# Performance work log

Hardware: AMD Instinct MI355X
Metric: run time of the kernel (lower is better)

## Reference

```python
import math
import jax, jax.numpy as jnp
import numpy as np

B, S, HID, NH = 2, 2048, 2048, 16
HD = HID // NH          # 128
QKD = HD // 2           # 64
BASE = 10000.0
LAYER_ID = 1
LAMBDA_INIT = 0.8 - 0.6 * math.exp(-0.3 * LAYER_ID)
EPS = 1e-6


def _rope_tables():
    i = np.arange(0, HD, 2, dtype=np.float32)
    theta = BASE ** (-i / HD)                      # [HD/2]
    pos = np.arange(S, dtype=np.float32)
    m_theta = np.outer(pos, theta)                 # [S, HD/2]
    cos = np.repeat(np.cos(m_theta), 2, axis=1)    # [S, HD]
    sin = np.repeat(np.sin(m_theta), 2, axis=1)
    return jnp.asarray(cos), jnp.asarray(sin)


def setup_inputs() -> dict:
    key = jax.random.key(0)
    ks = jax.random.split(key, 12)
    wstd = 0.02
    cos_emb, sin_emb = _rope_tables()
    return {
        "q": jax.random.normal(ks[0], (B, S, HID), jnp.float32),
        "k": jax.random.normal(ks[1], (B, S, HID), jnp.float32),
        "v": jax.random.normal(ks[2], (B, S, HID), jnp.float32),
        "Wq": jax.random.normal(ks[3], (HID, HID), jnp.float32) * wstd,
        "Wk": jax.random.normal(ks[4], (HID, HID), jnp.float32) * wstd,
        "Wv": jax.random.normal(ks[5], (HID, HID), jnp.float32) * wstd,
        "Wo": jax.random.normal(ks[6], (HID, HID), jnp.float32) * wstd,
        "lambda_q1": jax.random.normal(ks[7], (HD,), jnp.float32) * 0.1,
        "lambda_k1": jax.random.normal(ks[8], (HD,), jnp.float32) * 0.1,
        "lambda_q2": jax.random.normal(ks[9], (HD,), jnp.float32) * 0.1,
        "lambda_k2": jax.random.normal(ks[10], (HD,), jnp.float32) * 0.1,
        "gnorm_w": jnp.ones((HD,), jnp.float32),
        "cos_emb": cos_emb,
        "sin_emb": sin_emb,
        "mask": jnp.triu(jnp.ones((S, S), bool), 1),  # causal: True = masked
    }


def _apply_rope(x, cos_emb, sin_emb):
    # x: [B, 2, H, S, QKD]; tables sliced to [:S, :QKD] as in the torch code
    cos = cos_emb[:S, :QKD][None, None, None]
    sin = sin_emb[:S, :QKD][None, None, None]
    inv = jnp.stack((-x[..., 1::2], x[..., 0::2]), axis=-1).reshape(x.shape)
    return x * cos + inv * sin


def reference(q, k, v, Wq, Wk, Wv, Wo, lambda_q1, lambda_k1, lambda_q2,
              lambda_k2, gnorm_w, cos_emb, sin_emb, mask):
    lin = lambda x, W: jnp.einsum('bsi,oi->bso', x, W)  # torch Linear: x @ W.T
    qh = lin(q, Wq).reshape(B, S, NH, 2, QKD).transpose(0, 3, 2, 1, 4)  # [B,2,H,S,QKD]
    kh = lin(k, Wk).reshape(B, S, NH, 2, QKD).transpose(0, 3, 2, 1, 4)
    vh = lin(v, Wv).reshape(B, S, NH, HD).transpose(0, 2, 1, 3)          # [B,H,S,HD]
    qh = _apply_rope(qh, cos_emb, sin_emb)
    kh = _apply_rope(kh, cos_emb, sin_emb)

    scores = jnp.einsum('bghsd,bghtd->bghst', qh, kh) / math.sqrt(QKD)   # [B,2,H,S,S]
    scores = jnp.where(mask, jnp.finfo(jnp.float32).min, scores)

    lam1 = jnp.exp(jnp.sum(lambda_q1 * lambda_k1))
    lam2 = jnp.exp(jnp.sum(lambda_q2 * lambda_k2))
    lam = lam1 - lam2 + LAMBDA_INIT

    attn = jax.nn.softmax(scores[:, 0], axis=-1) - lam * jax.nn.softmax(scores[:, 1], axis=-1)
    out = jnp.einsum('bhst,bhtd->bhsd', attn, vh)                        # [B,H,S,HD]

    rms = out * jax.lax.rsqrt(jnp.mean(out * out, axis=-1, keepdims=True) + EPS) * gnorm_w
    out = (1.0 - LAMBDA_INIT) * rms
    out = out.transpose(0, 2, 1, 3).reshape(B, S, HID)
    return lin(out, Wo)
```

## Files before the change

kernel.cpp:

```cpp
#include <hip/hip_runtime.h>
#include <math.h>

#define BDIM 2
#define SDIM 2048
#define HIDD 2048
#define NHH 16
#define HDD 128
#define QKDD 64
#define MTOT (BDIM*SDIM)

constexpr float LAMBDA_INIT_F = 0.3555090675909693f;
constexpr float EPS_F = 1e-6f;
constexpr float SCALE2_F = 0.18033688011112042f;

typedef float f32x4 __attribute__((ext_vector_type(4)));
typedef short bf16x8 __attribute__((ext_vector_type(8)));
typedef short bf16x4 __attribute__((ext_vector_type(4)));

#define MFMA16(a, b, c) __builtin_amdgcn_mfma_f32_16x16x32_bf16((a), (b), (c), 0, 0, 0)

__device__ __forceinline__ short f2bf(float f) {
    unsigned u = __float_as_uint(f);
    u += 0x7FFFu + ((u >> 16) & 1u);
    return (short)(u >> 16);
}
__device__ __forceinline__ unsigned pk2(float a, float b) {
    return (unsigned)(unsigned short)f2bf(a) | ((unsigned)(unsigned short)f2bf(b) << 16);
}
__device__ __forceinline__ unsigned cvtpk(float lo, float hi) {
    unsigned r;
    asm("v_cvt_pk_bf16_f32 %0, %1, %2" : "=v"(r) : "v"(lo), "v"(hi));
    return r;
}

__device__ __forceinline__ void gload_lds16(const void* g, void* l) {
    __builtin_amdgcn_global_load_lds(
        (const __attribute__((address_space(1))) void*)g,
        (__attribute__((address_space(3))) void*)l, 16, 0, 0);
}
__device__ __forceinline__ void waitv8() { asm volatile("s_waitcnt vmcnt(8)" ::: "memory"); }
__device__ __forceinline__ void waitv0() { asm volatile("s_waitcnt vmcnt(0)" ::: "memory"); }
__device__ __forceinline__ void waitl0() { asm volatile("s_waitcnt lgkmcnt(0)" ::: "memory"); }
#define SBAR()   __builtin_amdgcn_s_barrier()
#define SCHEDB() __builtin_amdgcn_sched_barrier(0)

__global__ void lambda_kernel(const float* __restrict__ lq1, const float* __restrict__ lk1,
                              const float* __restrict__ lq2, const float* __restrict__ lk2,
                              float* __restrict__ lam_out) {
    int l = threadIdx.x;
    float d1 = lq1[l] * lk1[l] + lq1[l + 64] * lk1[l + 64];
    float d2 = lq2[l] * lk2[l] + lq2[l + 64] * lk2[l + 64];
#pragma unroll
    for (int o = 32; o > 0; o >>= 1) {
        d1 += __shfl_down(d1, o);
        d2 += __shfl_down(d2, o);
    }
    if (l == 0) lam_out[0] = expf(d1) - expf(d2) + LAMBDA_INIT_F;
}

__global__ __launch_bounds__(256) void conv_all(
        const float* __restrict__ q, const float* __restrict__ k,
        const float* __restrict__ v, const float* __restrict__ Wq,
        const float* __restrict__ Wk, const float* __restrict__ Wv,
        const float* __restrict__ Wo, short* __restrict__ xdst,
        short* __restrict__ wdst) {
    const size_t TEN_C = (size_t)1 << 23;
    const size_t WN_C  = (size_t)1 << 22;
    size_t i = ((size_t)blockIdx.x * 256 + threadIdx.x) * 8;
    const float* src;
    short* dst;
    size_t off;
    if (i < 3 * TEN_C) {
        int y = (int)(i >> 23);
        off = i & (TEN_C - 1);
        src = (y == 0) ? q : (y == 1) ? k : v;
        dst = xdst + ((size_t)y << 23);
    } else {
        size_t j = i - 3 * TEN_C;
        int y = (int)(j >> 22);
        off = j & (WN_C - 1);
        src = (y == 0) ? Wq : (y == 1) ? Wk : (y == 2) ? Wv : Wo;
        dst = wdst + ((size_t)y << 22);
    }
    float4 a = *(const float4*)&src[off];
    float4 b = *(const float4*)&src[off + 4];
    uint4 o;
    o.x = pk2(a.x, a.y); o.y = pk2(a.z, a.w);
    o.z = pk2(b.x, b.y); o.w = pk2(b.z, b.w);
    *(uint4*)&dst[off] = o;
}

#define GK 2048

__device__ __forceinline__ void gemm_mainloop(
        const short* __restrict__ X, const short* __restrict__ W,
        short* As, short* Bs, f32x4 acc[4][4],
        int bm, int bn, int w, int l, int lq, int lg, int wr, int wc) {
    const int scol = (((l & 7) ^ (l >> 3)) << 3);
    const int rsw  = (lq & 7) << 3;
    const short* aS[4]; const short* bS[4];
#pragma unroll
    for (int i = 0; i < 4; ++i) {
        const int c = w * 4 + i;
        aS[i] = X + (size_t)(bm + c * 8 + (l >> 3)) * GK + scol;
        bS[i] = W + (size_t)(bn + c * 8 + (l >> 3)) * GK + scol;
    }
    const int dOff = (w * 4) * 512;

#pragma unroll
    for (int i = 0; i < 4; ++i) {
        gload_lds16(aS[i], As + dOff + i * 512);
        gload_lds16(bS[i], Bs + dOff + i * 512);
    }
#pragma unroll
    for (int i = 0; i < 4; ++i) {
        gload_lds16(aS[i] + 64, As + 8192 + dOff + i * 512);
        gload_lds16(bS[i] + 64, Bs + 8192 + dOff + i * 512);
    }
    waitv8();
    SBAR();

    for (int t = 0; t < 30; ++t) {
        const short* Ab = As + (t & 1) * 8192;
        const short* Bb = Bs + (t & 1) * 8192;
        bf16x8 a[4][2], b[4][2];
#pragma unroll
        for (int m = 0; m < 4; ++m)
#pragma unroll
            for (int kk = 0; kk < 2; ++kk)
                a[m][kk] = *(const bf16x8*)&Ab[(wr * 64 + m * 16 + lq) * 64 + ((kk * 32 + lg * 8) ^ rsw)];
#pragma unroll
        for (int n = 0; n < 4; ++n)
#pragma unroll
            for (int kk = 0; kk < 2; ++kk)
                b[n][kk] = *(const bf16x8*)&Bb[(wc * 64 + n * 16 + lq) * 64 + ((kk * 32 + lg * 8) ^ rsw)];
        waitl0(); SCHEDB();
        SBAR();
        {
            short* Ad = As + (t & 1) * 8192 + dOff;
            short* Bd = Bs + (t & 1) * 8192 + dOff;
#pragma unroll
            for (int i = 0; i < 4; ++i) {
                gload_lds16(aS[i] + (t + 2) * 64, Ad + i * 512);
                gload_lds16(bS[i] + (t + 2) * 64, Bd + i * 512);
            }
        }
        SCHEDB();
#pragma unroll
        for (int kk = 0; kk < 2; ++kk)
#pragma unroll
            for (int m = 0; m < 4; ++m)
#pragma unroll
                for (int n = 0; n < 4; ++n)
                    acc[m][n] = MFMA16(a[m][kk], b[n][kk], acc[m][n]);
        waitv8();
        SBAR();
    }
    {
        bf16x8 a[4][2], b[4][2];
#pragma unroll
        for (int m = 0; m < 4; ++m)
#pragma unroll
            for (int kk = 0; kk < 2; ++kk)
                a[m][kk] = *(const bf16x8*)&As[(wr * 64 + m * 16 + lq) * 64 + ((kk * 32 + lg * 8) ^ rsw)];
#pragma unroll
        for (int n = 0; n < 4; ++n)
#pragma unroll
            for (int kk = 0; kk < 2; ++kk)
                b[n][kk] = *(const bf16x8*)&Bs[(wc * 64 + n * 16 + lq) * 64 + ((kk * 32 + lg * 8) ^ rsw)];
        waitl0(); SCHEDB();
        SBAR();
#pragma unroll
        for (int kk = 0; kk < 2; ++kk)
#pragma unroll
            for (int m = 0; m < 4; ++m)
#pragma unroll
                for (int n = 0; n < 4; ++n)
                    acc[m][n] = MFMA16(a[m][kk], b[n][kk], acc[m][n]);
        waitv0();
        SBAR();
    }
    {
        bf16x8 a[4][2], b[4][2];
#pragma unroll
        for (int m = 0; m < 4; ++m)
#pragma unroll
            for (int kk = 0; kk < 2; ++kk)
                a[m][kk] = *(const bf16x8*)&As[8192 + (wr * 64 + m * 16 + lq) * 64 + ((kk * 32 + lg * 8) ^ rsw)];
#pragma unroll
        for (int n = 0; n < 4; ++n)
#pragma unroll
            for (int kk = 0; kk < 2; ++kk)
                b[n][kk] = *(const bf16x8*)&Bs[8192 + (wc * 64 + n * 16 + lq) * 64 + ((kk * 32 + lg * 8) ^ rsw)];
#pragma unroll
        for (int kk = 0; kk < 2; ++kk)
#pragma unroll
            for (int m = 0; m < 4; ++m)
#pragma unroll
                for (int n = 0; n < 4; ++n)
                    acc[m][n] = MFMA16(a[m][kk], b[n][kk], acc[m][n]);
    }
}

__global__ __launch_bounds__(256) void qkv_gemm(
        const short* __restrict__ Xq, const short* __restrict__ Xk, const short* __restrict__ Xv,
        const short* __restrict__ Wb, short* __restrict__ Qb, short* __restrict__ Kb,
        short* __restrict__ Vb, const float* __restrict__ cosE, const float* __restrict__ sinE) {
    __shared__ short As[2 * 128 * 64];
    __shared__ short Bs[2 * 128 * 64];
    const int tid = threadIdx.x;
    const int w = tid >> 6, l = tid & 63;
    const int lq = l & 15, lg = l >> 4;
    const int wr = w >> 1, wc = w & 1;
    const int bm = blockIdx.y * 128;
    const int bn = blockIdx.x * 128;
    const int z  = blockIdx.z;

    const short* X = (z == 0) ? Xq : (z == 1) ? Xk : Xv;
    const short* W = Wb + (size_t)z * HIDD * HIDD;
    short* Cb      = (z == 0) ? Qb : (z == 1) ? Kb : Vb;

    f32x4 acc[4][4] = {};
    gemm_mainloop(X, W, As, Bs, acc, bm, bn, w, l, lq, lg, wr, wc);

    const bool dorope = (z < 2);
#pragma unroll
    for (int m = 0; m < 4; ++m)
#pragma unroll
        for (int n = 0; n < 4; ++n) {
            const int row0 = bm + wr * 64 + m * 16 + lg * 4;
            const int col  = bn + wc * 64 + n * 16 + lq;
#pragma unroll
            for (int r = 0; r < 4; ++r) {
                float vv = acc[m][n][r];
                if (dorope) {
                    const int s  = (row0 + r) & (SDIM - 1);
                    const int c6 = col & 63;
                    const float cv = cosE[s * HDD + c6];
                    const float sv = sinE[s * HDD + c6];
                    const float p = __shfl_xor(vv, 1);
                    vv = (col & 1) ? vv * cv + p * sv : vv * cv - p * sv;
                }
                Cb[(size_t)(row0 + r) * HIDD + col] = f2bf(vv);
            }
        }
}

__global__ __launch_bounds__(256) void o_gemm(const short* __restrict__ Ab,
                                              const short* __restrict__ Bb,
                                              float* __restrict__ C) {
    __shared__ short As[2 * 128 * 64];
    __shared__ short Bs[2 * 128 * 64];
    const int tid = threadIdx.x;
    const int w = tid >> 6, l = tid & 63;
    const int lq = l & 15, lg = l >> 4;
    const int wr = w >> 1, wc = w & 1;
    const int bm = blockIdx.y * 128;
    const int bn = blockIdx.x * 128;

    f32x4 acc[4][4] = {};
    gemm_mainloop(Ab, Bb, As, Bs, acc, bm, bn, w, l, lq, lg, wr, wc);

#pragma unroll
    for (int m = 0; m < 4; ++m)
#pragma unroll
        for (int n = 0; n < 4; ++n) {
            const int row0 = bm + wr * 64 + m * 16 + lg * 4;
            const int col  = bn + wc * 64 + n * 16 + lq;
#pragma unroll
            for (int r = 0; r < 4; ++r)
                C[(size_t)(row0 + r) * HIDD + col] = acc[m][n][r];
        }
}

#define KVB 64

__device__ __forceinline__ bf16x8 pack_pa(const float p0[4], const float p1[4]) {
    union { unsigned u[4]; bf16x8 v; } r;
    r.u[0] = cvtpk(p0[0], p0[1]);
    r.u[1] = cvtpk(p0[2], p0[3]);
    r.u[2] = cvtpk(p1[0], p1[1]);
    r.u[3] = cvtpk(p1[2], p1[3]);
    return r.v;
}

__device__ __forceinline__ void softmax_step(
        f32x4 sc[4], float& M, float& L, f32x4 O[8], bf16x8 pa[2],
        int t0, int qg, int lg, bool domask) {
#pragma unroll
    for (int sub = 0; sub < 4; ++sub)
#pragma unroll
        for (int r = 0; r < 4; ++r) {
            float s = sc[sub][r] * SCALE2_F;
            if (domask) {
                int key = t0 + sub * 16 + lg * 4 + r;
                s = (key <= qg) ? s : -1e30f;
            }
            sc[sub][r] = s;
        }
    float mx = -1e30f;
#pragma unroll
    for (int sub = 0; sub < 4; ++sub) {
        float a01 = fmaxf(sc[sub][0], sc[sub][1]);
        float a23 = fmaxf(sc[sub][2], sc[sub][3]);
        mx = fmaxf(mx, fmaxf(a01, a23));
    }
    mx = fmaxf(mx, __shfl_xor(mx, 16));
    mx = fmaxf(mx, __shfl_xor(mx, 32));
    if (__ballot(mx > M + 8.f)) {
        const float Mn = fmaxf(M, mx);
        const float a = __builtin_amdgcn_exp2f(M - Mn);
        M = Mn;
        L *= a;
        float ar[4];
#pragma unroll
        for (int r = 0; r < 4; ++r) ar[r] = __shfl(a, lg * 4 + r);
#pragma unroll
        for (int d = 0; d < 8; ++d) {
            O[d][0] *= ar[0]; O[d][1] *= ar[1]; O[d][2] *= ar[2]; O[d][3] *= ar[3];
        }
    }
    float p[4][4];
    float ps = 0.f;
#pragma unroll
    for (int sub = 0; sub < 4; ++sub) {
#pragma unroll
        for (int r = 0; r < 4; ++r) p[sub][r] = __builtin_amdgcn_exp2f(sc[sub][r] - M);
        ps += (p[sub][0] + p[sub][1]) + (p[sub][2] + p[sub][3]);
    }
    ps += __shfl_xor(ps, 16);
    ps += __shfl_xor(ps, 32);
    L += ps;
    pa[0] = pack_pa(p[0], p[1]);
    pa[1] = pack_pa(p[2], p[3]);
}

__global__ __launch_bounds__(256, 2) void flash_mfma(
        const short* __restrict__ Qb, const short* __restrict__ Kb,
        const short* __restrict__ Vb, const float* __restrict__ gnw,
        const float* __restrict__ lam_p, short* __restrict__ Hob) {
    __shared__ short Ksh[KVB * 128];
    __shared__ short VT[HDD * 72];

    const int tid = threadIdx.x;
    const int w  = tid >> 6;
    const int l  = tid & 63;
    const int lq = l & 15;
    const int lg = l >> 4;

    const int blk = blockIdx.x;
    const int bh  = blk & 31;
    const int g   = blk >> 5;
    const int r4  = g >> 3, gc = g & 7;
    const int bx  = (r4 == 0) ? 31 - gc : (r4 == 1) ? gc
                  : (r4 == 2) ? 23 - gc : 8 + gc;
    const int b = bh >> 4, h = bh & 15;
    const int s0 = bx * 64;
    const float lam = lam_p[0];

    const int qg = s0 + w * 16 + lq;
    const short* qrow = Qb + ((size_t)(b * SDIM + qg)) * HIDD + h * HDD;
    bf16x8 qf[2][2];
#pragma unroll
    for (int br = 0; br < 2; ++br)
#pragma unroll
        for (int ks = 0; ks < 2; ++ks)
            qf[br][ks] = *(const bf16x8*)(qrow + br * 64 + ks * 32 + lg * 8);

    int kkey[4], kcol[4];
#pragma unroll
    for (int i = 0; i < 4; ++i) {
        kkey[i] = w * 16 + i * 4 + lg;
        kcol[i] = (lq * 8) ^ ((kkey[i] & 7) << 3);
    }
    const int kp = tid & 31, dq = tid >> 5;

    const short* Kbase = Kb + ((size_t)(b * SDIM)) * HIDD + h * HDD;
    const short* Vbase = Vb + ((size_t)(b * SDIM)) * HIDD + h * HDD;

    float M1 = -1e30f, M2 = -1e30f, L1 = 0.f, L2 = 0.f;
    f32x4 O1[8] = {}; f32x4 O2[8] = {};

    const int ntmax = bx + 1;
    const int qmin = s0 + w * 16;

    for (int t = 0; t < ntmax; ++t) {
        const size_t trow = (size_t)t * KVB * HIDD;
        __syncthreads();
#pragma unroll
        for (int i = 0; i < 4; ++i)
            gload_lds16(Kbase + trow + (size_t)kkey[i] * HIDD + kcol[i],
                        &Ksh[w * 2048 + i * 512]);
        {
            const short* v0 = Vbase + trow + (size_t)(2 * kp) * HIDD + dq * 16;
            const short* v1 = v0 + HIDD;
            bf16x8 v00 = *(const bf16x8*)v0;
            bf16x8 v01 = *(const bf16x8*)(v0 + 8);
            bf16x8 v10 = *(const bf16x8*)v1;
            bf16x8 v11 = *(const bf16x8*)(v1 + 8);
#pragma unroll
            for (int j = 0; j < 8; ++j) {
                unsigned ua = (unsigned)(unsigned short)v00[j] |
                              ((unsigned)(unsigned short)v10[j] << 16);
                *(unsigned*)&VT[(dq * 16 + j) * 72 + 2 * kp] = ua;
                unsigned ub = (unsigned)(unsigned short)v01[j] |
                              ((unsigned)(unsigned short)v11[j] << 16);
                *(unsigned*)&VT[(dq * 16 + 8 + j) * 72 + 2 * kp] = ub;
            }
        }
        __syncthreads();

        f32x4 sc1[4] = {}; f32x4 sc2[4] = {};
        const int rsw = (lq & 7) << 3;
        __builtin_amdgcn_s_setprio(1);
#pragma unroll
        for (int sub = 0; sub < 4; ++sub) {
            const int rbase = (sub * 16 + lq) * 128;
            bf16x8 k00 = *(const bf16x8*)&Ksh[rbase + ((lg * 8) ^ rsw)];
            bf16x8 k01 = *(const bf16x8*)&Ksh[rbase + ((32 + lg * 8) ^ rsw)];
            bf16x8 k10 = *(const bf16x8*)&Ksh[rbase + ((64 + lg * 8) ^ rsw)];
            bf16x8 k11 = *(const bf16x8*)&Ksh[rbase + ((96 + lg * 8) ^ rsw)];
            sc1[sub] = MFMA16(k00, qf[0][0], sc1[sub]);
            sc1[sub] = MFMA16(k01, qf[0][1], sc1[sub]);
            sc2[sub] = MFMA16(k10, qf[1][0], sc2[sub]);
            sc2[sub] = MFMA16(k11, qf[1][1], sc2[sub]);
        }
        __builtin_amdgcn_s_setprio(0);
        const int t0 = t * KVB;
        const bool domask = (t0 + KVB - 1 > qmin);
        bf16x8 pa1[2], pa2[2];
        softmax_step(sc1, M1, L1, O1, pa1, t0, qg, lg, domask);
        softmax_step(sc2, M2, L2, O2, pa2, t0, qg, lg, domask);

        __builtin_amdgcn_s_setprio(1);
#pragma unroll
        for (int d0 = 0; d0 < 8; ++d0) {
            const short* vrow = &VT[(d0 * 16 + lq) * 72];
            bf16x4 a0 = *(const bf16x4*)&vrow[lg * 4];
            bf16x4 a1 = *(const bf16x4*)&vrow[16 + lg * 4];
            bf16x4 b0 = *(const bf16x4*)&vrow[32 + lg * 4];
            bf16x4 b1 = *(const bf16x4*)&vrow[48 + lg * 4];
            bf16x8 vb0 = __builtin_shufflevector(a0, a1, 0, 1, 2, 3, 4, 5, 6, 7);
            bf16x8 vb1 = __builtin_shufflevector(b0, b1, 0, 1, 2, 3, 4, 5, 6, 7);
            O1[d0] = MFMA16(pa1[0], vb0, O1[d0]);
            O1[d0] = MFMA16(pa1[1], vb1, O1[d0]);
            O2[d0] = MFMA16(pa2[0], vb0, O2[d0]);
            O2[d0] = MFMA16(pa2[1], vb1, O2[d0]);
        }
        __builtin_amdgcn_s_setprio(0);
    }

    const float inv1 = 1.f / L1;
    const float inv2 = lam / L2;
    float i1[4], i2[4];
#pragma unroll
    for (int r = 0; r < 4; ++r) {
        i1[r] = __shfl(inv1, lg * 4 + r);
        i2[r] = __shfl(inv2, lg * 4 + r);
    }
    float gn[8];
#pragma unroll
    for (int d = 0; d < 8; ++d) gn[d] = gnw[d * 16 + lq];
    float od[8][4];
    float ss[4] = {0.f, 0.f, 0.f, 0.f};
#pragma unroll
    for (int d = 0; d < 8; ++d)
#pragma unroll
        for (int r = 0; r < 4; ++r) {
            float o = O1[d][r] * i1[r] - O2[d][r] * i2[r];
            od[d][r] = o;
            ss[r] += o * o;
        }
#pragma unroll
    for (int r = 0; r < 4; ++r) {
        ss[r] += __shfl_xor(ss[r], 1);
        ss[r] += __shfl_xor(ss[r], 2);
        ss[r] += __shfl_xor(ss[r], 4);
        ss[r] += __shfl_xor(ss[r], 8);
    }
#pragma unroll
    for (int r = 0; r < 4; ++r) {
        const float scal = rsqrtf(ss[r] * (1.0f / HDD) + EPS_F) * (1.0f - LAMBDA_INIT_F);
        const size_t orow = ((size_t)(b * SDIM + s0 + w * 16 + lg * 4 + r)) * HIDD + h * HDD;
#pragma unroll
        for (int d = 0; d < 8; ++d)
            Hob[orow + d * 16 + lq] = f2bf(od[d][r] * scal * gn[d]);
    }
}

extern "C" void kernel_launch(void* const* d_in, const int* in_sizes, int n_in,
                              void* d_out, int out_size, void* d_ws, size_t ws_size,
                              hipStream_t stream) {
    const float* q   = (const float*)d_in[0];
    const float* k   = (const float*)d_in[1];
    const float* v   = (const float*)d_in[2];
    const float* Wq  = (const float*)d_in[3];
    const float* Wk  = (const float*)d_in[4];
    const float* Wv  = (const float*)d_in[5];
    const float* Wo  = (const float*)d_in[6];
    const float* lq1 = (const float*)d_in[7];
    const float* lk1 = (const float*)d_in[8];
    const float* lq2 = (const float*)d_in[9];
    const float* lk2 = (const float*)d_in[10];
    const float* gnw = (const float*)d_in[11];
    const float* cosE = (const float*)d_in[12];
    const float* sinE = (const float*)d_in[13];
    float* out = (float*)d_out;

    const size_t TEN = (size_t)BDIM * SDIM * HIDD;
    const int   WN  = HIDD * HIDD;

    short* wsS = (short*)d_ws;
    short* Qb   = wsS;
    short* Kb   = wsS + TEN;
    short* Vb   = wsS + 2 * TEN;
    short* xqkv = wsS + 3 * TEN;
    short* wb4  = wsS + 6 * TEN;
    float* lamp = (float*)(wsS + 6 * TEN + (size_t)4 * WN);
    short* Hob  = xqkv;

    lambda_kernel<<<1, 64, 0, stream>>>(lq1, lk1, lq2, lk2, lamp);

    conv_all<<<20480, 256, 0, stream>>>(q, k, v, Wq, Wk, Wv, Wo, xqkv, wb4);

    dim3 gq(HIDD / 128, MTOT / 128, 3);
    qkv_gemm<<<gq, 256, 0, stream>>>(xqkv, xqkv + TEN, xqkv + 2 * TEN, wb4,
                                     Qb, Kb, Vb, cosE, sinE);

    flash_mfma<<<(SDIM / 64) * BDIM * NHH, 256, 0, stream>>>(Qb, Kb, Vb, gnw, lamp, Hob);

    dim3 go(HIDD / 128, MTOT / 128);
    o_gemm<<<go, 256, 0, stream>>>(Hob, wb4 + (size_t)3 * WN, out);
}
```

Baseline: 302.9 us.

## Fuse lambda into conv, swizzle GEMM blocks, fold Q scale, widen V reads

Folds the lambda computation into an extra block of the conversion kernel, which removes one launch. Both GEMMs switch to a 1D grid with an XCD-aware block swizzle to improve L2 locality. The softmax scale is moved into the Q projection epilogue so the per-score multiply is gone. The transposed V tile is stored with a permuted key order so each MFMA operand can be read with one 8-wide LDS load instead of two 4-wide loads. The permutation must match the P fragment layout exactly, and scaling Q before the bf16 rounding slightly changes numerics.

```diff
diff --git a/kernel.cpp b/kernel.cpp
--- a/kernel.cpp
+++ b/kernel.cpp
@@ -44,26 +44,28 @@
 #define SBAR()   __builtin_amdgcn_s_barrier()
 #define SCHEDB() __builtin_amdgcn_sched_barrier(0)
 
-__global__ void lambda_kernel(const float* __restrict__ lq1, const float* __restrict__ lk1,
-                              const float* __restrict__ lq2, const float* __restrict__ lk2,
-                              float* __restrict__ lam_out) {
-    int l = threadIdx.x;
-    float d1 = lq1[l] * lk1[l] + lq1[l + 64] * lk1[l + 64];
-    float d2 = lq2[l] * lk2[l] + lq2[l + 64] * lk2[l + 64];
-#pragma unroll
-    for (int o = 32; o > 0; o >>= 1) {
-        d1 += __shfl_down(d1, o);
-        d2 += __shfl_down(d2, o);
-    }
-    if (l == 0) lam_out[0] = expf(d1) - expf(d2) + LAMBDA_INIT_F;
-}
-
 __global__ __launch_bounds__(256) void conv_all(
         const float* __restrict__ q, const float* __restrict__ k,
         const float* __restrict__ v, const float* __restrict__ Wq,
         const float* __restrict__ Wk, const float* __restrict__ Wv,
-        const float* __restrict__ Wo, short* __restrict__ xdst,
-        short* __restrict__ wdst) {
+        const float* __restrict__ Wo, const float* __restrict__ lq1,
+        const float* __restrict__ lk1, const float* __restrict__ lq2,
+        const float* __restrict__ lk2, short* __restrict__ xdst,
+        short* __restrict__ wdst, float* __restrict__ lam_out) {
+    if (blockIdx.x == 20480) {
+        int l = threadIdx.x;
+        if (l < 64) {
+            float d1 = lq1[l] * lk1[l] + lq1[l + 64] * lk1[l + 64];
+            float d2 = lq2[l] * lk2[l] + lq2[l + 64] * lk2[l + 64];
+#pragma unroll
+            for (int o = 32; o > 0; o >>= 1) {
+                d1 += __shfl_down(d1, o);
+                d2 += __shfl_down(d2, o);
+            }
+            if (l == 0) lam_out[0] = expf(d1) - expf(d2) + LAMBDA_INIT_F;
+        }
+        return;
+    }
     const size_t TEN_C = (size_t)1 << 23;
     const size_t WN_C  = (size_t)1 << 22;
     size_t i = ((size_t)blockIdx.x * 256 + threadIdx.x) * 8;
@@ -212,9 +214,13 @@
     const int w = tid >> 6, l = tid & 63;
     const int lq = l & 15, lg = l >> 4;
     const int wr = w >> 1, wc = w & 1;
-    const int bm = blockIdx.y * 128;
-    const int bn = blockIdx.x * 128;
-    const int z  = blockIdx.z;
+
+    const int bid = blockIdx.x;
+    const int swz = (bid & 7) * 192 + (bid >> 3);
+    const int z   = swz >> 9;
+    const int rr  = swz & 511;
+    const int bn  = (rr >> 5) * 128;
+    const int bm  = (rr & 31) * 128;
 
     const short* X = (z == 0) ? Xq : (z == 1) ? Xk : Xv;
     const short* W = Wb + (size_t)z * HIDD * HIDD;
@@ -224,6 +230,7 @@
     gemm_mainloop(X, W, As, Bs, acc, bm, bn, w, l, lq, lg, wr, wc);
 
     const bool dorope = (z < 2);
+    const float post = (z == 0) ? SCALE2_F : 1.0f;
 #pragma unroll
     for (int m = 0; m < 4; ++m)
 #pragma unroll
@@ -240,6 +247,7 @@
                     const float sv = sinE[s * HDD + c6];
                     const float p = __shfl_xor(vv, 1);
                     vv = (col & 1) ? vv * cv + p * sv : vv * cv - p * sv;
+                    vv *= post;
                 }
                 Cb[(size_t)(row0 + r) * HIDD + col] = f2bf(vv);
             }
@@ -255,8 +263,11 @@
     const int w = tid >> 6, l = tid & 63;
     const int lq = l & 15, lg = l >> 4;
     const int wr = w >> 1, wc = w & 1;
-    const int bm = blockIdx.y * 128;
-    const int bn = blockIdx.x * 128;
+
+    const int bid = blockIdx.x;
+    const int swz = (bid & 7) * 64 + (bid >> 3);
+    const int bn  = (swz >> 5) * 128;
+    const int bm  = (swz & 31) * 128;
 
     f32x4 acc[4][4] = {};
     gemm_mainloop(Ab, Bb, As, Bs, acc, bm, bn, w, l, lq, lg, wr, wc);
@@ -287,17 +298,15 @@
 __device__ __forceinline__ void softmax_step(
         f32x4 sc[4], float& M, float& L, f32x4 O[8], bf16x8 pa[2],
         int t0, int qg, int lg, bool domask) {
-#pragma unroll
-    for (int sub = 0; sub < 4; ++sub)
-#pragma unroll
-        for (int r = 0; r < 4; ++r) {
-            float s = sc[sub][r] * SCALE2_F;
-            if (domask) {
+    if (domask) {
+#pragma unroll
+        for (int sub = 0; sub < 4; ++sub)
+#pragma unroll
+            for (int r = 0; r < 4; ++r) {
                 int key = t0 + sub * 16 + lg * 4 + r;
-                s = (key <= qg) ? s : -1e30f;
+                if (key > qg) sc[sub][r] = -1e30f;
             }
-            sc[sub][r] = s;
-        }
+    }
     float mx = -1e30f;
 #pragma unroll
     for (int sub = 0; sub < 4; ++sub) {
@@ -374,6 +383,9 @@
         kcol[i] = (lq * 8) ^ ((kkey[i] & 7) << 3);
     }
     const int kp = tid & 31, dq = tid >> 5;
+    const int k0v = 2 * kp;
+    const int vp  = ((k0v >> 5) << 5) + (((k0v >> 2) & 3) << 3)
+                  + (((k0v >> 4) & 1) << 2) + (k0v & 3);
 
     const short* Kbase = Kb + ((size_t)(b * SDIM)) * HIDD + h * HDD;
     const short* Vbase = Vb + ((size_t)(b * SDIM)) * HIDD + h * HDD;
@@ -392,7 +404,7 @@
             gload_lds16(Kbase + trow + (size_t)kkey[i] * HIDD + kcol[i],
                         &Ksh[w * 2048 + i * 512]);
         {
-            const short* v0 = Vbase + trow + (size_t)(2 * kp) * HIDD + dq * 16;
+            const short* v0 = Vbase + trow + (size_t)k0v * HIDD + dq * 16;
             const short* v1 = v0 + HIDD;
             bf16x8 v00 = *(const bf16x8*)v0;
             bf16x8 v01 = *(const bf16x8*)(v0 + 8);
@@ -402,10 +414,10 @@
             for (int j = 0; j < 8; ++j) {
                 unsigned ua = (unsigned)(unsigned short)v00[j] |
                               ((unsigned)(unsigned short)v10[j] << 16);
-                *(unsigned*)&VT[(dq * 16 + j) * 72 + 2 * kp] = ua;
+                *(unsigned*)&VT[(dq * 16 + j) * 72 + vp] = ua;
                 unsigned ub = (unsigned)(unsigned short)v01[j] |
                               ((unsigned)(unsigned short)v11[j] << 16);
-                *(unsigned*)&VT[(dq * 16 + 8 + j) * 72 + 2 * kp] = ub;
+                *(unsigned*)&VT[(dq * 16 + 8 + j) * 72 + vp] = ub;
             }
         }
         __syncthreads();
@@ -436,12 +448,8 @@
 #pragma unroll
         for (int d0 = 0; d0 < 8; ++d0) {
             const short* vrow = &VT[(d0 * 16 + lq) * 72];
-            bf16x4 a0 = *(const bf16x4*)&vrow[lg * 4];
-            bf16x4 a1 = *(const bf16x4*)&vrow[16 + lg * 4];
-            bf16x4 b0 = *(const bf16x4*)&vrow[32 + lg * 4];
-            bf16x4 b1 = *(const bf16x4*)&vrow[48 + lg * 4];
-            bf16x8 vb0 = __builtin_shufflevector(a0, a1, 0, 1, 2, 3, 4, 5, 6, 7);
-            bf16x8 vb1 = __builtin_shufflevector(b0, b1, 0, 1, 2, 3, 4, 5, 6, 7);
+            bf16x8 vb0 = *(const bf16x8*)&vrow[lg * 8];
+            bf16x8 vb1 = *(const bf16x8*)&vrow[32 + lg * 8];
             O1[d0] = MFMA16(pa1[0], vb0, O1[d0]);
             O1[d0] = MFMA16(pa1[1], vb1, O1[d0]);
             O2[d0] = MFMA16(pa2[0], vb0, O2[d0]);
@@ -519,16 +527,13 @@
     float* lamp = (float*)(wsS + 6 * TEN + (size_t)4 * WN);
     short* Hob  = xqkv;
 
-    lambda_kernel<<<1, 64, 0, stream>>>(lq1, lk1, lq2, lk2, lamp);
-
-    conv_all<<<20480, 256, 0, stream>>>(q, k, v, Wq, Wk, Wv, Wo, xqkv, wb4);
-
-    dim3 gq(HIDD / 128, MTOT / 128, 3);
-    qkv_gemm<<<gq, 256, 0, stream>>>(xqkv, xqkv + TEN, xqkv + 2 * TEN, wb4,
-                                     Qb, Kb, Vb, cosE, sinE);
+    conv_all<<<20481, 256, 0, stream>>>(q, k, v, Wq, Wk, Wv, Wo,
+                                        lq1, lk1, lq2, lk2, xqkv, wb4, lamp);
+
+    qkv_gemm<<<1536, 256, 0, stream>>>(xqkv, xqkv + TEN, xqkv + 2 * TEN, wb4,
+                                       Qb, Kb, Vb, cosE, sinE);
 
     flash_mfma<<<(SDIM / 64) * BDIM * NHH, 256, 0, stream>>>(Qb, Kb, Vb, gnw, lamp, Hob);
 
-    dim3 go(HIDD / 128, MTOT / 128);
-    o_gemm<<<go, 256, 0, stream>>>(Hob, wb4 + (size_t)3 * WN, out);
-}
+    o_gemm<<<512, 256, 0, stream>>>(Hob, wb4 + (size_t)3 * WN, out);
+}
```

After: 338.6 us. 11.8% more time.
